# Performance work log

Hardware: AMD Instinct MI355X
Metric: run time of the kernel (lower is better)

The kernel has to match this reference:

```python
import jax, jax.numpy as jnp
import numpy as np

IN_DIM = 64  # in_dim, single head (num_heads=1)
SCALE = IN_DIM ** -0.5


def setup_inputs() -> dict:
    key = jax.random.key(0)
    k1, k2, k3 = jax.random.split(key, 3)
    B, N, C = 8, 3136, 147
    x = jax.random.normal(k1, (B, N, C), dtype=jnp.float32)
    # Linear weights stored pre-transposed: y = x @ W (+ b)
    W_qkv = jax.random.normal(k2, (C, 3 * IN_DIM), dtype=jnp.float32) * (C ** -0.5)
    W_proj = jax.random.normal(k3, (IN_DIM, IN_DIM), dtype=jnp.float32) * (IN_DIM ** -0.5)
    b_proj = jnp.zeros((IN_DIM,), dtype=jnp.float32)
    return {"x": x, "W_qkv": W_qkv, "W_proj": W_proj, "b_proj": b_proj}


def reference(x, W_qkv, W_proj, b_proj):
    B, N, C = x.shape
    qkv = (x @ W_qkv).reshape(B, N, 3, IN_DIM)  # [B, N, 3, D]
    q = qkv[:, :, 0]  # [B, N, D] (num_heads == 1)
    k = qkv[:, :, 1]
    v = qkv[:, :, 2]
    attn = jax.nn.softmax(jnp.einsum('bqd,bkd->bqk', q, k) * SCALE, axis=-1)  # [B, N, N]
    out = jnp.einsum('bqk,bkd->bqd', attn, v)  # [B, N, D]
    out = out @ W_proj + b_proj
    return v + out  # v-residual
```

## Files before the change

### kernel.cpp

```cpp
#include <hip/hip_runtime.h>

typedef short  bhalf8   __attribute__((ext_vector_type(8)));
typedef float  floatx16 __attribute__((ext_vector_type(16)));
typedef float  float4e  __attribute__((ext_vector_type(4)));

#define NTOK 3136
#define CDIM 147
#define NQT  98
#define KVT  49
#define NCHUNK 8
#define QTB  25
#define PARTB 4352

static __device__ __forceinline__ unsigned short f2bf(float f) {
    unsigned u = __float_as_uint(f);
    u += 0x7fffu + ((u >> 16) & 1u);
    return (unsigned short)(u >> 16);
}
static __device__ __forceinline__ float bf2f(unsigned short h) {
    return __uint_as_float(((unsigned)h) << 16);
}
static __device__ __forceinline__ unsigned packbf2(float a, float b) {
    unsigned r;
    asm("v_cvt_pk_bf16_f32 %0, %1, %2" : "=v"(r) : "v"(a), "v"(b));
    return r;
}
static __device__ __forceinline__ float fexp2(float x) {
#if __has_builtin(__builtin_amdgcn_exp2f)
    return __builtin_amdgcn_exp2f(x);
#else
    return __expf(x * 0.69314718056f);
#endif
}

__global__ __launch_bounds__(256) void prep_w_kernel(
    const float* __restrict__ W, unsigned short* __restrict__ WbT)
{
    const int idx = blockIdx.x * 256 + threadIdx.x;
    if (idx >= 192 * 160) return;
    const int c = idx / 160, k = idx - c * 160;
    WbT[idx] = (k < CDIM) ? f2bf(W[(size_t)k * 192 + c]) : (unsigned short)0;
}

__global__ __launch_bounds__(384) void qkv_mfma_kernel(
    const float* __restrict__ x, const unsigned short* __restrict__ WbT,
    unsigned short* __restrict__ qb, unsigned short* __restrict__ kb,
    unsigned short* __restrict__ vT)
{
    __shared__ __align__(16) unsigned char xls[32 * 384];
    const int tid = threadIdx.x;
    const int wave = tid >> 6, lane = tid & 63;
    const int l31 = lane & 31, hi = lane >> 5;
    const int n0g = blockIdx.x * 32;
    const int b = n0g / NTOK, nn0 = n0g - b * NTOK;

    for (int i = tid; i < 640; i += 384) {
        const int row = i / 20, c = i - row * 20;
        const float* src = x + (size_t)(n0g + row) * CDIM + c * 8;
        float f[8];
        if (c < 18) {
            const float4e a = *reinterpret_cast<const float4e*>(src);
            const float4e v2 = *reinterpret_cast<const float4e*>(src + 4);
            f[0]=a[0]; f[1]=a[1]; f[2]=a[2]; f[3]=a[3];
            f[4]=v2[0]; f[5]=v2[1]; f[6]=v2[2]; f[7]=v2[3];
        } else if (c == 18) {
            f[0]=src[0]; f[1]=src[1]; f[2]=src[2];
            f[3]=f[4]=f[5]=f[6]=f[7]=0.f;
        } else {
            f[0]=f[1]=f[2]=f[3]=f[4]=f[5]=f[6]=f[7]=0.f;
        }
        uint4 u;
        u.x = packbf2(f[0], f[1]); u.y = packbf2(f[2], f[3]);
        u.z = packbf2(f[4], f[5]); u.w = packbf2(f[6], f[7]);
        const int phys = (c & ~7) | ((c & 7) ^ (row & 7));
        *reinterpret_cast<uint4*>(&xls[row * 384 + phys * 16]) = u;
    }
    __syncthreads();

    const int wcol = wave * 32;
    const bhalf8* wrow = reinterpret_cast<const bhalf8*>(WbT + (size_t)(wcol + l31) * 160);
    floatx16 acc;
#pragma unroll
    for (int r = 0; r < 16; ++r) acc[r] = 0.f;

    if (wave < 4) {
#pragma unroll
        for (int s = 0; s < 10; ++s) {
            const int slot = 2 * s + hi;
            const int phys = (slot & ~7) | ((slot & 7) ^ (l31 & 7));
            const bhalf8 xf = *reinterpret_cast<const bhalf8*>(&xls[l31 * 384 + phys * 16]);
            acc = __builtin_amdgcn_mfma_f32_32x32x16_bf16(xf, wrow[slot], acc, 0, 0, 0);
        }
        unsigned short* dst = (wave < 2) ? qb : kb;
        const int c0 = (wave & 1) * 32 + l31;
#pragma unroll
        for (int r = 0; r < 16; ++r) {
            const int n = n0g + (r & 3) + 8 * (r >> 2) + 4 * hi;
            dst[(size_t)n * 64 + c0] = f2bf(acc[r]);
        }
    } else {
#pragma unroll
        for (int s = 0; s < 10; ++s) {
            const int slot = 2 * s + hi;
            const int phys = (slot & ~7) | ((slot & 7) ^ (l31 & 7));
            const bhalf8 xf = *reinterpret_cast<const bhalf8*>(&xls[l31 * 384 + phys * 16]);
            acc = __builtin_amdgcn_mfma_f32_32x32x16_bf16(wrow[slot], xf, acc, 0, 0, 0);
        }
        const int nc = nn0 + l31;
#pragma unroll
        for (int r = 0; r < 16; ++r) {
            const int c = (wave - 4) * 32 + (r & 3) + 8 * (r >> 2) + 4 * hi;
            vT[((size_t)b * 64 + c) * NTOK + nc] = f2bf(acc[r]);
        }
    }
}

static __device__ __forceinline__ bhalf8 build_frag(unsigned a0, unsigned a1,
                                                    unsigned a2, unsigned a3, int hi)
{
    const unsigned py1 = __shfl_xor(hi ? a0 : a2, 32);
    const unsigned py2 = __shfl_xor(hi ? a1 : a3, 32);
    union { unsigned w[4]; bhalf8 v; } f;
    f.w[0] = hi ? py1 : a0;
    f.w[1] = hi ? py2 : a1;
    f.w[2] = hi ? a2 : py1;
    f.w[3] = hi ? a3 : py2;
    return f.v;
}

static __device__ __forceinline__ void attn_epilogue(
    const floatx16& accO0, const floatx16& accO1, float inv,
    const float* __restrict__ Wp, const float* __restrict__ bp,
    const unsigned short* __restrict__ vb, float* __restrict__ orow,
    int q, int l31, int hi)
{
    unsigned ok0[8], ok1[8];
#pragma unroll
    for (int w = 0; w < 8; ++w) {
        ok0[w] = packbf2(accO0[2 * w] * inv, accO0[2 * w + 1] * inv);
        ok1[w] = packbf2(accO1[2 * w] * inv, accO1[2 * w + 1] * inv);
    }
    floatx16 accP0, accP1;
#pragma unroll
    for (int r = 0; r < 16; ++r) { accP0[r] = 0.f; accP1[r] = 0.f; }
#pragma unroll
    for (int ks = 0; ks < 4; ++ks) {
        const int t = ks & 1;
        const bhalf8 of = (ks >> 1) ? build_frag(ok1[4*t], ok1[4*t+1], ok1[4*t+2], ok1[4*t+3], hi)
                                    : build_frag(ok0[4*t], ok0[4*t+1], ok0[4*t+2], ok0[4*t+3], hi);
        union { unsigned w[4]; bhalf8 v; } wa, wb;
#pragma unroll
        for (int jj = 0; jj < 4; ++jj) {
            const int d0 = 16 * ks + 8 * hi + 2 * jj;
            wa.w[jj] = packbf2(Wp[(size_t)d0 * 64 + l31],      Wp[(size_t)(d0 + 1) * 64 + l31]);
            wb.w[jj] = packbf2(Wp[(size_t)d0 * 64 + 32 + l31], Wp[(size_t)(d0 + 1) * 64 + 32 + l31]);
        }
        accP0 = __builtin_amdgcn_mfma_f32_32x32x16_bf16(wa.v, of, accP0, 0, 0, 0);
        accP1 = __builtin_amdgcn_mfma_f32_32x32x16_bf16(wb.v, of, accP1, 0, 0, 0);
    }
#pragma unroll
    for (int r = 0; r < 16; ++r) {
        const int e0 = (r & 3) + 8 * (r >> 2) + 4 * hi;
        const int e1 = e0 + 32;
        const float va = bf2f(vb[(size_t)e0 * NTOK + q]);
        const float vc = bf2f(vb[(size_t)e1 * NTOK + q]);
        orow[(size_t)q * 64 + e0] = accP0[r] + bp[e0] + va;
        orow[(size_t)q * 64 + e1] = accP1[r] + bp[e1] + vc;
    }
}

__global__ __launch_bounds__(256) void attn_split_kernel(
    const unsigned short* __restrict__ qb,
    const unsigned short* __restrict__ kbf,
    const unsigned short* __restrict__ vT,
    char* __restrict__ part)
{
    __shared__ __align__(16) unsigned char lds[2][16384];
    const int tid  = threadIdx.x;
    const int wave = tid >> 6, lane = tid & 63;
    const int l31 = lane & 31, hi = lane >> 5;
    const int qtb = blockIdx.x, b = blockIdx.y, ck = blockIdx.z;
    int qt = qtb * 4 + wave; if (qt >= NQT) qt = NQT - 1;
    const size_t bofs = (size_t)b * NTOK * 64;
    const int q0 = qt * 32;
    const float SM = 0.125f * 1.44269504f;

    const bhalf8* qrow = reinterpret_cast<const bhalf8*>(qb + bofs + (size_t)(q0 + l31) * 64);
    bhalf8 Qf[4];
#pragma unroll
    for (int s = 0; s < 4; ++s) Qf[s] = qrow[2 * s + hi];

    floatx16 accO0, accO1;
#pragma unroll
    for (int r = 0; r < 16; ++r) { accO0[r] = 0.f; accO1[r] = 0.f; }
    float lsum = 0.f;

    const unsigned short* vb = vT + (size_t)b * 64 * NTOK;
    const int kv_lo = (ck * KVT) / NCHUNK;
    const int kv_hi = ((ck + 1) * KVT) / NCHUNK;

    const int r0 = tid >> 3,  s0i = tid & 7;
    const int r1 = r0 + 32;
    const int swz0 = (s0i ^ (r0 & 7)) << 4;
    uint4 rK0, rK1, rV0, rV1;

#define STAGE_LOAD(kvt_) do {                                                   \
        const uint4* ks_ = reinterpret_cast<const uint4*>(                      \
            kbf + bofs + (size_t)(kvt_) * 64 * 64);                             \
        rK0 = ks_[tid]; rK1 = ks_[tid + 256];                                   \
        rV0 = *reinterpret_cast<const uint4*>(                                  \
            vb + (size_t)r0 * NTOK + (kvt_) * 64 + s0i * 8);                    \
        rV1 = *reinterpret_cast<const uint4*>(                                  \
            vb + (size_t)r1 * NTOK + (kvt_) * 64 + s0i * 8);                    \
    } while (0)

#define STAGE_WRITE(buf_) do {                                                  \
        *reinterpret_cast<uint4*>(&lds[buf_][r0 * 128 + swz0])          = rK0;  \
        *reinterpret_cast<uint4*>(&lds[buf_][r1 * 128 + swz0])          = rK1;  \
        *reinterpret_cast<uint4*>(&lds[buf_][8192 + r0 * 128 + swz0])   = rV0;  \
        *reinterpret_cast<uint4*>(&lds[buf_][8192 + r1 * 128 + swz0])   = rV1;  \
    } while (0)

    STAGE_LOAD(kv_lo);
    int buf = 0;
    const int kswz = (l31 & 7);
    for (int kvt = kv_lo; kvt < kv_hi; ++kvt) {
        STAGE_WRITE(buf);
        if (kvt + 1 < kv_hi) STAGE_LOAD(kvt + 1);
        __syncthreads();

        floatx16 s0, s1;
#pragma unroll
        for (int r = 0; r < 16; ++r) { s0[r] = 0.f; s1[r] = 0.f; }
#pragma unroll
        for (int s = 0; s < 4; ++s) {
            const int sl = ((2 * s + hi) ^ kswz) << 4;
            const bhalf8 kf0 = *reinterpret_cast<const bhalf8*>(&lds[buf][l31 * 128 + sl]);
            const bhalf8 kf1 = *reinterpret_cast<const bhalf8*>(&lds[buf][(32 + l31) * 128 + sl]);
            s0 = __builtin_amdgcn_mfma_f32_32x32x16_bf16(kf0, Qf[s], s0, 0, 0, 0);
            s1 = __builtin_amdgcn_mfma_f32_32x32x16_bf16(kf1, Qf[s], s1, 0, 0, 0);
        }
        float ps0 = 0.f, ps1 = 0.f;
#pragma unroll
        for (int r = 0; r < 16; ++r) {
            const float p0 = fexp2(s0[r] * SM); s0[r] = p0;
            const float p1 = fexp2(s1[r] * SM); s1[r] = p1;
            ps0 += p0; ps1 += p1;
        }
        lsum += ps0 + ps1;
        unsigned pk0[8], pk1[8];
#pragma unroll
        for (int w = 0; w < 8; ++w) {
            pk0[w] = packbf2(s0[2 * w], s0[2 * w + 1]);
            pk1[w] = packbf2(s1[2 * w], s1[2 * w + 1]);
        }
#pragma unroll
        for (int u = 0; u < 2; ++u) {
#pragma unroll
            for (int t = 0; t < 2; ++t) {
                const bhalf8 pf = u ? build_frag(pk1[4*t], pk1[4*t+1], pk1[4*t+2], pk1[4*t+3], hi)
                                    : build_frag(pk0[4*t], pk0[4*t+1], pk0[4*t+2], pk0[4*t+3], hi);
                const int sl = ((4 * u + 2 * t + hi) ^ kswz) << 4;
                const bhalf8 v0 = *reinterpret_cast<const bhalf8*>(&lds[buf][8192 + l31 * 128 + sl]);
                const bhalf8 v1 = *reinterpret_cast<const bhalf8*>(&lds[buf][8192 + (32 + l31) * 128 + sl]);
                accO0 = __builtin_amdgcn_mfma_f32_32x32x16_bf16(v0, pf, accO0, 0, 0, 0);
                accO1 = __builtin_amdgcn_mfma_f32_32x32x16_bf16(v1, pf, accO1, 0, 0, 0);
            }
        }
        buf ^= 1;
    }
#undef STAGE_LOAD
#undef STAGE_WRITE

    char* pbb = part + ((size_t)(b * NQT + qt) * NCHUNK + ck) * PARTB;
#pragma unroll
    for (int rg = 0; rg < 4; ++rg) {
        uint2 w0, w1;
        w0.x = packbf2(accO0[4*rg],     accO0[4*rg + 1]);
        w0.y = packbf2(accO0[4*rg + 2], accO0[4*rg + 3]);
        w1.x = packbf2(accO1[4*rg],     accO1[4*rg + 1]);
        w1.y = packbf2(accO1[4*rg + 2], accO1[4*rg + 3]);
        *reinterpret_cast<uint2*>(pbb + (rg * 64 + lane) * 8)        = w0;
        *reinterpret_cast<uint2*>(pbb + 2048 + (rg * 64 + lane) * 8) = w1;
    }
    *reinterpret_cast<float*>(pbb + 4096 + lane * 4) = lsum;
}

__global__ __launch_bounds__(256) void attn_combine_kernel(
    const char* __restrict__ part,
    const unsigned short* __restrict__ vT,
    const float* __restrict__ Wp, const float* __restrict__ bp,
    float* __restrict__ out)
{
    const int wid  = blockIdx.x * 4 + (threadIdx.x >> 6);
    const int lane = threadIdx.x & 63;
    const int qt   = wid % NQT;
    const int b    = wid / NQT;
    const int l31 = lane & 31, hi = lane >> 5;
    const char* pbase = part + (size_t)(b * NQT + qt) * NCHUNK * PARTB;

    floatx16 accO0, accO1;
#pragma unroll
    for (int r = 0; r < 16; ++r) { accO0[r] = 0.f; accO1[r] = 0.f; }
    float lsum = 0.f;
#pragma unroll
    for (int c = 0; c < NCHUNK; ++c) {
        const char* pbb = pbase + (size_t)c * PARTB;
#pragma unroll
        for (int rg = 0; rg < 4; ++rg) {
            const uint2 u0 = *reinterpret_cast<const uint2*>(pbb + (rg * 64 + lane) * 8);
            const uint2 u1 = *reinterpret_cast<const uint2*>(pbb + 2048 + (rg * 64 + lane) * 8);
            accO0[4*rg]     += __uint_as_float(u0.x << 16);
            accO0[4*rg + 1] += __uint_as_float(u0.x & 0xffff0000u);
            accO0[4*rg + 2] += __uint_as_float(u0.y << 16);
            accO0[4*rg + 3] += __uint_as_float(u0.y & 0xffff0000u);
            accO1[4*rg]     += __uint_as_float(u1.x << 16);
            accO1[4*rg + 1] += __uint_as_float(u1.x & 0xffff0000u);
            accO1[4*rg + 2] += __uint_as_float(u1.y << 16);
            accO1[4*rg + 3] += __uint_as_float(u1.y & 0xffff0000u);
        }
        lsum += *reinterpret_cast<const float*>(pbb + 4096 + lane * 4);
    }
    const float L = lsum + __shfl_xor(lsum, 32);
    const unsigned short* vb = vT + (size_t)b * 64 * NTOK;
    attn_epilogue(accO0, accO1, 1.0f / L, Wp, bp, vb, out + (size_t)b * NTOK * 64,
                  qt * 32 + l31, l31, hi);
}

__global__ __launch_bounds__(64) void attn_kernel(
    const unsigned short* __restrict__ qb,
    const unsigned short* __restrict__ kbf,
    const unsigned short* __restrict__ vT,
    const float* __restrict__ Wp, const float* __restrict__ bp,
    float* __restrict__ out)
{
    const int qt = blockIdx.x, b = blockIdx.y;
    const int lane = threadIdx.x;
    const int l31 = lane & 31, hi = lane >> 5;
    const size_t bofs = (size_t)b * NTOK * 64;
    const int q0 = qt * 32;
    const float SM = 0.125f * 1.44269504f;

    const bhalf8* qrow = reinterpret_cast<const bhalf8*>(qb + bofs + (size_t)(q0 + l31) * 64);
    bhalf8 Qf[4];
#pragma unroll
    for (int s = 0; s < 4; ++s) Qf[s] = qrow[2 * s + hi];

    floatx16 accO0, accO1;
#pragma unroll
    for (int r = 0; r < 16; ++r) { accO0[r] = 0.f; accO1[r] = 0.f; }
    float lsum = 0.f;
    const unsigned short* vb = vT + (size_t)b * 64 * NTOK;
    for (int kvt = 0; kvt < KVT; ++kvt) {
        const int kv0 = kvt * 64;
        const bhalf8* kr0 = reinterpret_cast<const bhalf8*>(kbf + bofs + (size_t)(kv0 + l31) * 64);
        const bhalf8* kr1 = reinterpret_cast<const bhalf8*>(kbf + bofs + (size_t)(kv0 + 32 + l31) * 64);
        floatx16 s0, s1;
#pragma unroll
        for (int r = 0; r < 16; ++r) { s0[r] = 0.f; s1[r] = 0.f; }
#pragma unroll
        for (int s = 0; s < 4; ++s) {
            s0 = __builtin_amdgcn_mfma_f32_32x32x16_bf16(kr0[2 * s + hi], Qf[s], s0, 0, 0, 0);
            s1 = __builtin_amdgcn_mfma_f32_32x32x16_bf16(kr1[2 * s + hi], Qf[s], s1, 0, 0, 0);
        }
        float ps0 = 0.f, ps1 = 0.f;
#pragma unroll
        for (int r = 0; r < 16; ++r) {
            const float p0 = fexp2(s0[r] * SM); s0[r] = p0;
            const float p1 = fexp2(s1[r] * SM); s1[r] = p1;
            ps0 += p0; ps1 += p1;
        }
        lsum += ps0 + ps1;
        unsigned pk0[8], pk1[8];
#pragma unroll
        for (int w = 0; w < 8; ++w) {
            pk0[w] = packbf2(s0[2 * w], s0[2 * w + 1]);
            pk1[w] = packbf2(s1[2 * w], s1[2 * w + 1]);
        }
#pragma unroll
        for (int u = 0; u < 2; ++u) {
#pragma unroll
            for (int t = 0; t < 2; ++t) {
                const bhalf8 pf = u ? build_frag(pk1[4*t], pk1[4*t+1], pk1[4*t+2], pk1[4*t+3], hi)
                                    : build_frag(pk0[4*t], pk0[4*t+1], pk0[4*t+2], pk0[4*t+3], hi);
                const int col = kv0 + 32 * u + 16 * t + 8 * hi;
                const bhalf8 v0 = *reinterpret_cast<const bhalf8*>(vb + (size_t)l31 * NTOK + col);
                const bhalf8 v1 = *reinterpret_cast<const bhalf8*>(vb + (size_t)(32 + l31) * NTOK + col);
                accO0 = __builtin_amdgcn_mfma_f32_32x32x16_bf16(v0, pf, accO0, 0, 0, 0);
                accO1 = __builtin_amdgcn_mfma_f32_32x32x16_bf16(v1, pf, accO1, 0, 0, 0);
            }
        }
    }
    const float L = lsum + __shfl_xor(lsum, 32);
    attn_epilogue(accO0, accO1, 1.0f / L, Wp, bp, vb, out + bofs,
                  q0 + l31, l31, hi);
}

extern "C" void kernel_launch(void* const* d_in, const int* in_sizes, int n_in,
                              void* d_out, int out_size, void* d_ws, size_t ws_size,
                              hipStream_t stream)
{
    const float* x  = (const float*)d_in[0];
    const float* Wq = (const float*)d_in[1];
    const float* Wp = (const float*)d_in[2];
    const float* bp = (const float*)d_in[3];
    float* out = (float*)d_out;

    unsigned short* qbuf = (unsigned short*)d_ws;
    unsigned short* kbuf = qbuf + (size_t)8 * NTOK * 64;
    unsigned short* vTb  = kbuf + (size_t)8 * NTOK * 64;
    const size_t bf_bytes = (size_t)3 * 8 * NTOK * 64 * 2;
    char* part = (char*)d_ws + bf_bytes;
    const size_t part_bytes = (size_t)8 * NQT * NCHUNK * PARTB;
    unsigned short* WbT = (unsigned short*)((char*)d_ws + bf_bytes + part_bytes);
    const size_t need = bf_bytes + part_bytes + 192 * 160 * 2;

    if (ws_size >= need) {
        prep_w_kernel<<<dim3(120), 256, 0, stream>>>(Wq, WbT);
        qkv_mfma_kernel<<<dim3(8 * NTOK / 32), 384, 0, stream>>>(x, WbT, qbuf, kbuf, vTb);
        attn_split_kernel<<<dim3(QTB, 8, NCHUNK), 256, 0, stream>>>(qbuf, kbuf, vTb, part);
        attn_combine_kernel<<<dim3(8 * NQT / 4), 256, 0, stream>>>(part, vTb, Wp, bp, out);
    } else {
        prep_w_kernel<<<dim3(120), 256, 0, stream>>>(Wq, (unsigned short*)part);
        qkv_mfma_kernel<<<dim3(8 * NTOK / 32), 384, 0, stream>>>(x, (unsigned short*)part, qbuf, kbuf, vTb);
        attn_kernel<<<dim3(NQT, 8), 64, 0, stream>>>(qbuf, kbuf, vTb, Wp, bp, out);
    }
}
```

Measured before the change: 64.64 us.

## Fold softmax scale into Q projection and single-buffer LDS in split attention

Multiplies Q by the softmax scale times log2e when writing it from the QKV kernel, removing a per-score multiply before exp2 in both attention kernels. The split attention kernel also drops double-buffered LDS for a single 16KB buffer, refilled between two barriers each iteration. This halves LDS use, possibly allowing more resident blocks, but adds a barrier per tile and exposes global-to-LDS latency. Scaling before the bf16 rounding slightly changes numerics.

```diff
diff --git a/kernel.cpp b/kernel.cpp
--- a/kernel.cpp
+++ b/kernel.cpp
@@ -53,6 +53,7 @@
     const int l31 = lane & 31, hi = lane >> 5;
     const int n0g = blockIdx.x * 32;
     const int b = n0g / NTOK, nn0 = n0g - b * NTOK;
+    const float SM = 0.125f * 1.44269504f;
 
     for (int i = tid; i < 640; i += 384) {
         const int row = i / 20, c = i - row * 20;
@@ -92,11 +93,12 @@
             acc = __builtin_amdgcn_mfma_f32_32x32x16_bf16(xf, wrow[slot], acc, 0, 0, 0);
         }
         unsigned short* dst = (wave < 2) ? qb : kb;
+        const float scl = (wave < 2) ? SM : 1.0f;
         const int c0 = (wave & 1) * 32 + l31;
 #pragma unroll
         for (int r = 0; r < 16; ++r) {
             const int n = n0g + (r & 3) + 8 * (r >> 2) + 4 * hi;
-            dst[(size_t)n * 64 + c0] = f2bf(acc[r]);
+            dst[(size_t)n * 64 + c0] = f2bf(acc[r] * scl);
         }
     } else {
 #pragma unroll
@@ -175,7 +177,7 @@
     const unsigned short* __restrict__ vT,
     char* __restrict__ part)
 {
-    __shared__ __align__(16) unsigned char lds[2][16384];
+    __shared__ __align__(16) unsigned char lds[16384];
     const int tid  = threadIdx.x;
     const int wave = tid >> 6, lane = tid & 63;
     const int l31 = lane & 31, hi = lane >> 5;
@@ -183,7 +185,6 @@
     int qt = qtb * 4 + wave; if (qt >= NQT) qt = NQT - 1;
     const size_t bofs = (size_t)b * NTOK * 64;
     const int q0 = qt * 32;
-    const float SM = 0.125f * 1.44269504f;
 
     const bhalf8* qrow = reinterpret_cast<const bhalf8*>(qb + bofs + (size_t)(q0 + l31) * 64);
     bhalf8 Qf[4];
@@ -214,20 +215,20 @@
             vb + (size_t)r1 * NTOK + (kvt_) * 64 + s0i * 8);                    \
     } while (0)
 
-#define STAGE_WRITE(buf_) do {                                                  \
-        *reinterpret_cast<uint4*>(&lds[buf_][r0 * 128 + swz0])          = rK0;  \
-        *reinterpret_cast<uint4*>(&lds[buf_][r1 * 128 + swz0])          = rK1;  \
-        *reinterpret_cast<uint4*>(&lds[buf_][8192 + r0 * 128 + swz0])   = rV0;  \
-        *reinterpret_cast<uint4*>(&lds[buf_][8192 + r1 * 128 + swz0])   = rV1;  \
+#define STAGE_WRITE() do {                                                      \
+        *reinterpret_cast<uint4*>(&lds[r0 * 128 + swz0])          = rK0;        \
+        *reinterpret_cast<uint4*>(&lds[r1 * 128 + swz0])          = rK1;        \
+        *reinterpret_cast<uint4*>(&lds[8192 + r0 * 128 + swz0])   = rV0;        \
+        *reinterpret_cast<uint4*>(&lds[8192 + r1 * 128 + swz0])   = rV1;        \
     } while (0)
 
     STAGE_LOAD(kv_lo);
-    int buf = 0;
+    STAGE_WRITE();
+    __syncthreads();
     const int kswz = (l31 & 7);
     for (int kvt = kv_lo; kvt < kv_hi; ++kvt) {
-        STAGE_WRITE(buf);
-        if (kvt + 1 < kv_hi) STAGE_LOAD(kvt + 1);
-        __syncthreads();
+        const bool more = (kvt + 1 < kv_hi);
+        if (more) STAGE_LOAD(kvt + 1);
 
         floatx16 s0, s1;
 #pragma unroll
@@ -235,16 +236,16 @@
 #pragma unroll
         for (int s = 0; s < 4; ++s) {
             const int sl = ((2 * s + hi) ^ kswz) << 4;
-            const bhalf8 kf0 = *reinterpret_cast<const bhalf8*>(&lds[buf][l31 * 128 + sl]);
-            const bhalf8 kf1 = *reinterpret_cast<const bhalf8*>(&lds[buf][(32 + l31) * 128 + sl]);
+            const bhalf8 kf0 = *reinterpret_cast<const bhalf8*>(&lds[l31 * 128 + sl]);
+            const bhalf8 kf1 = *reinterpret_cast<const bhalf8*>(&lds[(32 + l31) * 128 + sl]);
             s0 = __builtin_amdgcn_mfma_f32_32x32x16_bf16(kf0, Qf[s], s0, 0, 0, 0);
             s1 = __builtin_amdgcn_mfma_f32_32x32x16_bf16(kf1, Qf[s], s1, 0, 0, 0);
         }
         float ps0 = 0.f, ps1 = 0.f;
 #pragma unroll
         for (int r = 0; r < 16; ++r) {
-            const float p0 = fexp2(s0[r] * SM); s0[r] = p0;
-            const float p1 = fexp2(s1[r] * SM); s1[r] = p1;
+            const float p0 = fexp2(s0[r]); s0[r] = p0;
+            const float p1 = fexp2(s1[r]); s1[r] = p1;
             ps0 += p0; ps1 += p1;
         }
         lsum += ps0 + ps1;
@@ -261,13 +262,17 @@
                 const bhalf8 pf = u ? build_frag(pk1[4*t], pk1[4*t+1], pk1[4*t+2], pk1[4*t+3], hi)
                                     : build_frag(pk0[4*t], pk0[4*t+1], pk0[4*t+2], pk0[4*t+3], hi);
                 const int sl = ((4 * u + 2 * t + hi) ^ kswz) << 4;
-                const bhalf8 v0 = *reinterpret_cast<const bhalf8*>(&lds[buf][8192 + l31 * 128 + sl]);
-                const bhalf8 v1 = *reinterpret_cast<const bhalf8*>(&lds[buf][8192 + (32 + l31) * 128 + sl]);
+                const bhalf8 v0 = *reinterpret_cast<const bhalf8*>(&lds[8192 + l31 * 128 + sl]);
+                const bhalf8 v1 = *reinterpret_cast<const bhalf8*>(&lds[8192 + (32 + l31) * 128 + sl]);
                 accO0 = __builtin_amdgcn_mfma_f32_32x32x16_bf16(v0, pf, accO0, 0, 0, 0);
                 accO1 = __builtin_amdgcn_mfma_f32_32x32x16_bf16(v1, pf, accO1, 0, 0, 0);
             }
         }
-        buf ^= 1;
+        if (more) {
+            __syncthreads();
+            STAGE_WRITE();
+            __syncthreads();
+        }
     }
 #undef STAGE_LOAD
 #undef STAGE_WRITE
@@ -339,7 +344,6 @@
     const int l31 = lane & 31, hi = lane >> 5;
     const size_t bofs = (size_t)b * NTOK * 64;
     const int q0 = qt * 32;
-    const float SM = 0.125f * 1.44269504f;
 
     const bhalf8* qrow = reinterpret_cast<const bhalf8*>(qb + bofs + (size_t)(q0 + l31) * 64);
     bhalf8 Qf[4];
@@ -366,8 +370,8 @@
         float ps0 = 0.f, ps1 = 0.f;
 #pragma unroll
         for (int r = 0; r < 16; ++r) {
-            const float p0 = fexp2(s0[r] * SM); s0[r] = p0;
-            const float p1 = fexp2(s1[r] * SM); s1[r] = p1;
+            const float p0 = fexp2(s0[r]); s0[r] = p0;
+            const float p1 = fexp2(s1[r]); s1[r] = p1;
             ps0 += p0; ps1 += p1;
         }
         lsum += ps0 + ps1;
```

After: 64.72 us. Within noise of the previous version (+0.1%).

## Fold softmax scale into Q and widen attention blocks to eight waves

Applied to the files above, without the earlier changes.

Moves the softmax scale and log2e factor into the QKV projection so Q is stored pre-scaled, which removes a multiply per score in the attention loops. The split attention kernel now runs 512 threads (8 query tiles per block) over 13 blocks in x, so each K/V tile staged in LDS is shared by twice as many waves and each thread stages half as much. The first score MFMA now starts from a zero vector instead of a re-zeroed accumulator. Rounding Q to bf16 after scaling slightly changes numerics, and the larger blocks may cut occupancy or leave the last block with duplicate clamped tiles.

```diff
diff --git a/kernel.cpp b/kernel.cpp
--- a/kernel.cpp
+++ b/kernel.cpp
@@ -9,7 +9,7 @@
 #define NQT  98
 #define KVT  49
 #define NCHUNK 8
-#define QTB  25
+#define QTB8 13
 #define PARTB 4352
 
 static __device__ __forceinline__ unsigned short f2bf(float f) {
@@ -53,6 +53,7 @@
     const int l31 = lane & 31, hi = lane >> 5;
     const int n0g = blockIdx.x * 32;
     const int b = n0g / NTOK, nn0 = n0g - b * NTOK;
+    const float SM = 0.125f * 1.44269504f;
 
     for (int i = tid; i < 640; i += 384) {
         const int row = i / 20, c = i - row * 20;
@@ -92,11 +93,12 @@
             acc = __builtin_amdgcn_mfma_f32_32x32x16_bf16(xf, wrow[slot], acc, 0, 0, 0);
         }
         unsigned short* dst = (wave < 2) ? qb : kb;
+        const float scl = (wave < 2) ? SM : 1.0f;
         const int c0 = (wave & 1) * 32 + l31;
 #pragma unroll
         for (int r = 0; r < 16; ++r) {
             const int n = n0g + (r & 3) + 8 * (r >> 2) + 4 * hi;
-            dst[(size_t)n * 64 + c0] = f2bf(acc[r]);
+            dst[(size_t)n * 64 + c0] = f2bf(acc[r] * scl);
         }
     } else {
 #pragma unroll
@@ -169,7 +171,7 @@
     }
 }
 
-__global__ __launch_bounds__(256) void attn_split_kernel(
+__global__ __launch_bounds__(512) void attn_split_kernel(
     const unsigned short* __restrict__ qb,
     const unsigned short* __restrict__ kbf,
     const unsigned short* __restrict__ vT,
@@ -180,19 +182,18 @@
     const int wave = tid >> 6, lane = tid & 63;
     const int l31 = lane & 31, hi = lane >> 5;
     const int qtb = blockIdx.x, b = blockIdx.y, ck = blockIdx.z;
-    int qt = qtb * 4 + wave; if (qt >= NQT) qt = NQT - 1;
+    int qt = qtb * 8 + wave; if (qt >= NQT) qt = NQT - 1;
     const size_t bofs = (size_t)b * NTOK * 64;
     const int q0 = qt * 32;
-    const float SM = 0.125f * 1.44269504f;
 
     const bhalf8* qrow = reinterpret_cast<const bhalf8*>(qb + bofs + (size_t)(q0 + l31) * 64);
     bhalf8 Qf[4];
 #pragma unroll
     for (int s = 0; s < 4; ++s) Qf[s] = qrow[2 * s + hi];
 
-    floatx16 accO0, accO1;
-#pragma unroll
-    for (int r = 0; r < 16; ++r) { accO0[r] = 0.f; accO1[r] = 0.f; }
+    floatx16 accO0, accO1, z16;
+#pragma unroll
+    for (int r = 0; r < 16; ++r) { accO0[r] = 0.f; accO1[r] = 0.f; z16[r] = 0.f; }
     float lsum = 0.f;
 
     const unsigned short* vb = vT + (size_t)b * 64 * NTOK;
@@ -200,25 +201,19 @@
     const int kv_hi = ((ck + 1) * KVT) / NCHUNK;
 
     const int r0 = tid >> 3,  s0i = tid & 7;
-    const int r1 = r0 + 32;
     const int swz0 = (s0i ^ (r0 & 7)) << 4;
-    uint4 rK0, rK1, rV0, rV1;
+    uint4 rK, rV;
 
 #define STAGE_LOAD(kvt_) do {                                                   \
-        const uint4* ks_ = reinterpret_cast<const uint4*>(                      \
-            kbf + bofs + (size_t)(kvt_) * 64 * 64);                             \
-        rK0 = ks_[tid]; rK1 = ks_[tid + 256];                                   \
-        rV0 = *reinterpret_cast<const uint4*>(                                  \
+        rK = reinterpret_cast<const uint4*>(                                    \
+            kbf + bofs + (size_t)(kvt_) * 64 * 64)[tid];                        \
+        rV = *reinterpret_cast<const uint4*>(                                   \
             vb + (size_t)r0 * NTOK + (kvt_) * 64 + s0i * 8);                    \
-        rV1 = *reinterpret_cast<const uint4*>(                                  \
-            vb + (size_t)r1 * NTOK + (kvt_) * 64 + s0i * 8);                    \
     } while (0)
 
 #define STAGE_WRITE(buf_) do {                                                  \
-        *reinterpret_cast<uint4*>(&lds[buf_][r0 * 128 + swz0])          = rK0;  \
-        *reinterpret_cast<uint4*>(&lds[buf_][r1 * 128 + swz0])          = rK1;  \
-        *reinterpret_cast<uint4*>(&lds[buf_][8192 + r0 * 128 + swz0])   = rV0;  \
-        *reinterpret_cast<uint4*>(&lds[buf_][8192 + r1 * 128 + swz0])   = rV1;  \
+        *reinterpret_cast<uint4*>(&lds[buf_][r0 * 128 + swz0])        = rK;     \
+        *reinterpret_cast<uint4*>(&lds[buf_][8192 + r0 * 128 + swz0]) = rV;     \
     } while (0)
 
     STAGE_LOAD(kv_lo);
@@ -230,10 +225,15 @@
         __syncthreads();
 
         floatx16 s0, s1;
-#pragma unroll
-        for (int r = 0; r < 16; ++r) { s0[r] = 0.f; s1[r] = 0.f; }
-#pragma unroll
-        for (int s = 0; s < 4; ++s) {
+        {
+            const int sl = (hi ^ kswz) << 4;
+            const bhalf8 kf0 = *reinterpret_cast<const bhalf8*>(&lds[buf][l31 * 128 + sl]);
+            const bhalf8 kf1 = *reinterpret_cast<const bhalf8*>(&lds[buf][(32 + l31) * 128 + sl]);
+            s0 = __builtin_amdgcn_mfma_f32_32x32x16_bf16(kf0, Qf[0], z16, 0, 0, 0);
+            s1 = __builtin_amdgcn_mfma_f32_32x32x16_bf16(kf1, Qf[0], z16, 0, 0, 0);
+        }
+#pragma unroll
+        for (int s = 1; s < 4; ++s) {
             const int sl = ((2 * s + hi) ^ kswz) << 4;
             const bhalf8 kf0 = *reinterpret_cast<const bhalf8*>(&lds[buf][l31 * 128 + sl]);
             const bhalf8 kf1 = *reinterpret_cast<const bhalf8*>(&lds[buf][(32 + l31) * 128 + sl]);
@@ -243,8 +243,8 @@
         float ps0 = 0.f, ps1 = 0.f;
 #pragma unroll
         for (int r = 0; r < 16; ++r) {
-            const float p0 = fexp2(s0[r] * SM); s0[r] = p0;
-            const float p1 = fexp2(s1[r] * SM); s1[r] = p1;
+            const float p0 = fexp2(s0[r]); s0[r] = p0;
+            const float p1 = fexp2(s1[r]); s1[r] = p1;
             ps0 += p0; ps1 += p1;
         }
         lsum += ps0 + ps1;
@@ -339,7 +339,6 @@
     const int l31 = lane & 31, hi = lane >> 5;
     const size_t bofs = (size_t)b * NTOK * 64;
     const int q0 = qt * 32;
-    const float SM = 0.125f * 1.44269504f;
 
     const bhalf8* qrow = reinterpret_cast<const bhalf8*>(qb + bofs + (size_t)(q0 + l31) * 64);
     bhalf8 Qf[4];
@@ -366,8 +365,8 @@
         float ps0 = 0.f, ps1 = 0.f;
 #pragma unroll
         for (int r = 0; r < 16; ++r) {
-            const float p0 = fexp2(s0[r] * SM); s0[r] = p0;
-            const float p1 = fexp2(s1[r] * SM); s1[r] = p1;
+            const float p0 = fexp2(s0[r]); s0[r] = p0;
+            const float p1 = fexp2(s1[r]); s1[r] = p1;
             ps0 += p0; ps1 += p1;
         }
         lsum += ps0 + ps1;
@@ -418,7 +417,7 @@
     if (ws_size >= need) {
         prep_w_kernel<<<dim3(120), 256, 0, stream>>>(Wq, WbT);
         qkv_mfma_kernel<<<dim3(8 * NTOK / 32), 384, 0, stream>>>(x, WbT, qbuf, kbuf, vTb);
-        attn_split_kernel<<<dim3(QTB, 8, NCHUNK), 256, 0, stream>>>(qbuf, kbuf, vTb, part);
+        attn_split_kernel<<<dim3(QTB8, 8, NCHUNK), 512, 0, stream>>>(qbuf, kbuf, vTb, part);
         attn_combine_kernel<<<dim3(8 * NQT / 4), 256, 0, stream>>>(part, vTb, Wp, bp, out);
     } else {
         prep_w_kernel<<<dim3(120), 256, 0, stream>>>(Wq, (unsigned short*)part);
```

Result: faster. 60.61 us (-6.2%).
